# Optimization experiments

Hardware: AMD Instinct MI355X
Metric: run time of the kernel (lower is better)

The kernel has to match this reference:

```python
import jax, jax.numpy as jnp
import numpy as np

EPS = 1e-06


def elu_plus_one(x):
    # F.elu(x) + 1 == exp(x) for x < 0, x + 1 for x >= 0 (alpha=1)
    return jnp.where(x > 0, x + 1.0, jnp.exp(jnp.minimum(x, 0.0)))


def safe_divide(a, b, eps=EPS):
    return a / (b + eps)


def setup_inputs() -> dict:
    key0 = jax.random.key(0)
    kq, kk, kv, kM, kz = jax.random.split(key0, 5)
    B, H, S, D = 4, 16, 4096, 128
    query = jax.random.normal(kq, (B, H, S, D), dtype=jnp.float32)
    key = jax.random.normal(kk, (B, H, S, D), dtype=jnp.float32)
    value = jax.random.normal(kv, (B, H, S, D), dtype=jnp.float32)
    M = jax.random.normal(kM, (B, H, D, D), dtype=jnp.float32)
    z = jax.random.uniform(kz, (B, H, D, 1), dtype=jnp.float32)
    return {"query": query, "key": key, "value": value, "M": M, "z": z}


def reference(query, key, value, M, z):
    # --- update (delta rule) ---
    sigma_k = elu_plus_one(key)                       # [B,H,S,D]
    mem_pred = jnp.einsum('bhsd,bhde->bhse', sigma_k, M)   # sigma(K) @ M
    normalizer = jnp.einsum('bhsd,bhdo->bhso', sigma_k, z) # sigma(K) @ z -> [B,H,S,1]
    delta_v = value - safe_divide(mem_pred, normalizer)
    M_new = M + jnp.einsum('bhsd,bhse->bhde', sigma_k, delta_v)  # sigma(K)^T @ delta_V
    z_new = z + jnp.sum(sigma_k, axis=2)[..., None]              # [B,H,D,1]

    # --- retrieve with updated memory ---
    sigma_q = elu_plus_one(query)
    mem_out = jnp.einsum('bhsd,bhde->bhse', sigma_q, M_new)
    norm_q = jnp.einsum('bhsd,bhdo->bhso', sigma_q, z_new)
    out = safe_divide(mem_out, norm_q)                # [B,H,S,D]
    return out, M_new, z_new
```

## Files before the change

kernel.cpp:

```cpp
#include <hip/hip_runtime.h>
#include <math.h>

#define D 128
#define EPS 1e-6f
#define SKR_LD 136
#define SKT_LD 40

typedef __attribute__((ext_vector_type(8))) short short8;
typedef __attribute__((ext_vector_type(4))) float f32x4;
typedef unsigned short ushort_t;
typedef unsigned long long u64;

__device__ __forceinline__ float elu1(float x) {
    float e = __expf(fminf(x, 0.f));
    return x > 0.f ? x + 1.f : e;
}
__device__ __forceinline__ unsigned short bf16rne(float f) {
    unsigned u = __builtin_bit_cast(unsigned, f);
    u += 0x7FFFu + ((u >> 16) & 1u);
    return (unsigned short)(u >> 16);
}
__device__ __forceinline__ u64 pack4(float a, float b, float c, float d) {
    return (u64)bf16rne(a) | ((u64)bf16rne(b) << 16) |
           ((u64)bf16rne(c) << 32) | ((u64)bf16rne(d) << 48);
}

__global__ __launch_bounds__(256, 2)
void k_update(const float* __restrict__ key, const float* __restrict__ value,
              const float* __restrict__ M, const float* __restrict__ z,
              float* __restrict__ pM, float* __restrict__ pz, int S)
{
    __shared__ alignas(16) ushort_t skR[2][32 * SKR_LD];
    __shared__ alignas(16) ushort_t skT[2][128 * SKT_LD];
    __shared__ float normsh[2][32];
    __shared__ float zsc[8][128];

    const int t  = threadIdx.x;
    const int bh = blockIdx.x, ch = blockIdx.y, NCH = gridDim.y;
    const int SC = S / NCH;
    const int NB = SC / 32;
    const int s0g = ch * SC;

    const int w = t >> 6, g = (t >> 4) & 3, m = t & 15;
    const int sb = t >> 5, db = t & 31;

    const float* Kb = key   + (size_t)bh * S * D;
    const float* Vb = value + (size_t)bh * S * D;
    const float* Mb = M + (size_t)bh * D * D;
    const float* zb = z + (size_t)bh * D;

    float zr[4];
    #pragma unroll
    for (int j = 0; j < 4; ++j) zr[j] = zb[4 * db + j];

    short8 Bf[4][2];
    #pragma unroll
    for (int ks = 0; ks < 4; ++ks)
        #pragma unroll
        for (int p = 0; p < 2; ++p) {
            short8 f;
            #pragma unroll
            for (int j = 0; j < 8; ++j)
                f[j] = (short)bf16rne(Mb[(size_t)(32 * ks + 8 * g + j) * D + 16 * (2 * w + p) + m]);
            Bf[ks][p] = f;
        }

    f32x4 acc[8][2];
    #pragma unroll
    for (int dt = 0; dt < 8; ++dt)
        #pragma unroll
        for (int p = 0; p < 2; ++p) acc[dt][p] = 0.f;
    float zp[4] = {0.f, 0.f, 0.f, 0.f};

    auto STAGE_PROC = [&](const float4* kreg, int bu) {
        float sv[4][4];
        #pragma unroll
        for (int js = 0; js < 4; ++js) {
            sv[js][0] = elu1(kreg[js].x); sv[js][1] = elu1(kreg[js].y);
            sv[js][2] = elu1(kreg[js].z); sv[js][3] = elu1(kreg[js].w);
        }
        #pragma unroll
        for (int js = 0; js < 4; ++js)
            *(u64*)&skR[bu][(4 * sb + js) * SKR_LD + 4 * db] =
                pack4(sv[js][0], sv[js][1], sv[js][2], sv[js][3]);
        #pragma unroll
        for (int jd = 0; jd < 4; ++jd)
            *(u64*)&skT[bu][(4 * db + jd) * SKT_LD + 4 * sb] =
                pack4(sv[0][jd], sv[1][jd], sv[2][jd], sv[3][jd]);
        float np[4];
        #pragma unroll
        for (int js = 0; js < 4; ++js) {
            np[js] = sv[js][0] * zr[0] + sv[js][1] * zr[1] +
                     sv[js][2] * zr[2] + sv[js][3] * zr[3];
            #pragma unroll
            for (int jd = 0; jd < 4; ++jd) zp[jd] += sv[js][jd];
        }
        #pragma unroll
        for (int mask = 16; mask >= 1; mask >>= 1) {
            np[0] += __shfl_xor(np[0], mask, 64);
            np[1] += __shfl_xor(np[1], mask, 64);
            np[2] += __shfl_xor(np[2], mask, 64);
            np[3] += __shfl_xor(np[3], mask, 64);
        }
        if (db < 4) {
            float v = db == 0 ? np[0] : db == 1 ? np[1] : db == 2 ? np[2] : np[3];
            normsh[bu][4 * sb + db] = v + EPS;
        }
    };

    {
        float4 kreg[4];
        #pragma unroll
        for (int js = 0; js < 4; ++js)
            kreg[js] = *(const float4*)&Kb[(size_t)(s0g + 4 * sb + js) * D + 4 * db];
        STAGE_PROC(kreg, 0);
    }
    __syncthreads();

    for (int b = 0; b < NB; ++b) {
        const int bu = b & 1;
        float vv[2][2][4];
        #pragma unroll
        for (int st = 0; st < 2; ++st)
            #pragma unroll
            for (int p = 0; p < 2; ++p)
                #pragma unroll
                for (int r = 0; r < 4; ++r)
                    vv[st][p][r] = Vb[(size_t)(s0g + 32 * b + 16 * st + 4 * g + r) * D +
                                      16 * (2 * w + p) + m];
        float4 kreg[4];
        if (b + 1 < NB) {
            #pragma unroll
            for (int js = 0; js < 4; ++js)
                kreg[js] = *(const float4*)&Kb[(size_t)(s0g + 32 * (b + 1) + 4 * sb + js) * D + 4 * db];
        }

        f32x4 mp[2][2];
        #pragma unroll
        for (int st = 0; st < 2; ++st)
            #pragma unroll
            for (int p = 0; p < 2; ++p) mp[st][p] = 0.f;
        #pragma unroll
        for (int st = 0; st < 2; ++st)
            #pragma unroll
            for (int ks = 0; ks < 4; ++ks) {
                short8 a = *(short8*)&skR[bu][(16 * st + m) * SKR_LD + 32 * ks + 8 * g];
                #pragma unroll
                for (int p = 0; p < 2; ++p)
                    mp[st][p] = __builtin_amdgcn_mfma_f32_16x16x32_bf16(a, Bf[ks][p], mp[st][p], 0, 0, 0);
            }

        float dvv[2][2][4];
        #pragma unroll
        for (int st = 0; st < 2; ++st)
            #pragma unroll
            for (int r = 0; r < 4; ++r) {
                float nrm = normsh[bu][16 * st + 4 * g + r];
                #pragma unroll
                for (int p = 0; p < 2; ++p)
                    dvv[st][p][r] = vv[st][p][r] - mp[st][p][r] / nrm;
            }

        short8 bfr[2];
        #pragma unroll
        for (int p = 0; p < 2; ++p) {
            short8 f;
            #pragma unroll
            for (int j = 0; j < 8; ++j) {
                int src = ((2 * g + (j >> 2)) & 3) * 16 + m;
                float v0 = __shfl(dvv[0][p][j & 3], src, 64);
                float v1 = __shfl(dvv[1][p][j & 3], src, 64);
                f[j] = (short)bf16rne(g < 2 ? v0 : v1);
            }
            bfr[p] = f;
        }

        #pragma unroll
        for (int dt = 0; dt < 8; ++dt) {
            short8 a = *(short8*)&skT[bu][(16 * dt + m) * SKT_LD + 8 * g];
            #pragma unroll
            for (int p = 0; p < 2; ++p)
                acc[dt][p] = __builtin_amdgcn_mfma_f32_16x16x32_bf16(a, bfr[p], acc[dt][p], 0, 0, 0);
        }

        if (b + 1 < NB) STAGE_PROC(kreg, (b + 1) & 1);
        __syncthreads();
    }

    float* pMb = pM + ((size_t)bh * NCH + ch) * (D * D);
    #pragma unroll
    for (int dt = 0; dt < 8; ++dt)
        #pragma unroll
        for (int p = 0; p < 2; ++p)
            #pragma unroll
            for (int r = 0; r < 4; ++r)
                pMb[(size_t)(16 * dt + 4 * g + r) * D + 16 * (2 * w + p) + m] = acc[dt][p][r];

    #pragma unroll
    for (int jd = 0; jd < 4; ++jd) zsc[sb][4 * db + jd] = zp[jd];
    __syncthreads();
    if (t < 128) {
        float a = 0.f;
        #pragma unroll
        for (int q = 0; q < 8; ++q) a += zsc[q][t];
        pz[((size_t)bh * NCH + ch) * D + t] = a;
    }
}

__global__ void k_reduce(const float* __restrict__ M, const float* __restrict__ z,
                         const float* __restrict__ pM, const float* __restrict__ pz,
                         float* __restrict__ Mnew, float* __restrict__ znew, int NCH)
{
    const int bh = blockIdx.x, sl = blockIdx.y, t = threadIdx.x;
    const size_t baseM = (size_t)bh * D * D;
    for (int i = sl * 2048 + t; i < (sl + 1) * 2048; i += 256) {
        float a = M[baseM + i];
        for (int c = 0; c < NCH; ++c) a += pM[((size_t)bh * NCH + c) * (D * D) + i];
        Mnew[baseM + i] = a;
    }
    if (sl == 0 && t < D) {
        float a = z[(size_t)bh * D + t];
        for (int c = 0; c < NCH; ++c) a += pz[((size_t)bh * NCH + c) * D + t];
        znew[(size_t)bh * D + t] = a;
    }
}

__global__ __launch_bounds__(256, 2)
void k_retrieve(const float* __restrict__ query, const float* __restrict__ Mnew,
                const float* __restrict__ znew, float* __restrict__ out, int S)
{
    __shared__ alignas(16) ushort_t sqR[2][32 * SKR_LD];
    __shared__ float normsh[2][32];

    const int t  = threadIdx.x;
    const int bh = blockIdx.x, ch = blockIdx.y, NCH = gridDim.y;
    const int SC = S / NCH;
    const int NB = SC / 32;
    const int s0g = ch * SC;

    const int w = t >> 6, g = (t >> 4) & 3, m = t & 15;
    const int sb = t >> 5, db = t & 31;

    const float* Qb = query + (size_t)bh * S * D;
    const float* Mb = Mnew + (size_t)bh * D * D;
    const float* zb = znew + (size_t)bh * D;
    float*       Ob = out + (size_t)bh * S * D;

    float zr[4];
    #pragma unroll
    for (int j = 0; j < 4; ++j) zr[j] = zb[4 * db + j];

    short8 Bf[4][2];
    #pragma unroll
    for (int ks = 0; ks < 4; ++ks)
        #pragma unroll
        for (int p = 0; p < 2; ++p) {
            short8 f;
            #pragma unroll
            for (int j = 0; j < 8; ++j)
                f[j] = (short)bf16rne(Mb[(size_t)(32 * ks + 8 * g + j) * D + 16 * (2 * w + p) + m]);
            Bf[ks][p] = f;
        }

    auto STAGE_PROC = [&](const float4* qreg, int bu) {
        float sv[4][4];
        #pragma unroll
        for (int js = 0; js < 4; ++js) {
            sv[js][0] = elu1(qreg[js].x); sv[js][1] = elu1(qreg[js].y);
            sv[js][2] = elu1(qreg[js].z); sv[js][3] = elu1(qreg[js].w);
        }
        #pragma unroll
        for (int js = 0; js < 4; ++js)
            *(u64*)&sqR[bu][(4 * sb + js) * SKR_LD + 4 * db] =
                pack4(sv[js][0], sv[js][1], sv[js][2], sv[js][3]);
        float np[4];
        #pragma unroll
        for (int js = 0; js < 4; ++js)
            np[js] = sv[js][0] * zr[0] + sv[js][1] * zr[1] +
                     sv[js][2] * zr[2] + sv[js][3] * zr[3];
        #pragma unroll
        for (int mask = 16; mask >= 1; mask >>= 1) {
            np[0] += __shfl_xor(np[0], mask, 64);
            np[1] += __shfl_xor(np[1], mask, 64);
            np[2] += __shfl_xor(np[2], mask, 64);
            np[3] += __shfl_xor(np[3], mask, 64);
        }
        if (db < 4) {
            float v = db == 0 ? np[0] : db == 1 ? np[1] : db == 2 ? np[2] : np[3];
            normsh[bu][4 * sb + db] = v + EPS;
        }
    };

    {
        float4 qreg[4];
        #pragma unroll
        for (int js = 0; js < 4; ++js)
            qreg[js] = *(const float4*)&Qb[(size_t)(s0g + 4 * sb + js) * D + 4 * db];
        STAGE_PROC(qreg, 0);
    }
    __syncthreads();

    for (int b = 0; b < NB; ++b) {
        const int bu = b & 1;
        float4 qreg[4];
        if (b + 1 < NB) {
            #pragma unroll
            for (int js = 0; js < 4; ++js)
                qreg[js] = *(const float4*)&Qb[(size_t)(s0g + 32 * (b + 1) + 4 * sb + js) * D + 4 * db];
        }

        f32x4 mp[2][2];
        #pragma unroll
        for (int st = 0; st < 2; ++st)
            #pragma unroll
            for (int p = 0; p < 2; ++p) mp[st][p] = 0.f;
        #pragma unroll
        for (int st = 0; st < 2; ++st)
            #pragma unroll
            for (int ks = 0; ks < 4; ++ks) {
                short8 a = *(short8*)&sqR[bu][(16 * st + m) * SKR_LD + 32 * ks + 8 * g];
                #pragma unroll
                for (int p = 0; p < 2; ++p)
                    mp[st][p] = __builtin_amdgcn_mfma_f32_16x16x32_bf16(a, Bf[ks][p], mp[st][p], 0, 0, 0);
            }

        #pragma unroll
        for (int st = 0; st < 2; ++st)
            #pragma unroll
            for (int r = 0; r < 4; ++r) {
                float rn = 1.f / normsh[bu][16 * st + 4 * g + r];
                #pragma unroll
                for (int p = 0; p < 2; ++p)
                    Ob[(size_t)(s0g + 32 * b + 16 * st + 4 * g + r) * D + 16 * (2 * w + p) + m] =
                        mp[st][p][r] * rn;
            }

        if (b + 1 < NB) STAGE_PROC(qreg, (b + 1) & 1);
        __syncthreads();
    }
}

extern "C" void kernel_launch(void* const* d_in, const int* in_sizes, int n_in,
                              void* d_out, int out_size, void* d_ws, size_t ws_size,
                              hipStream_t stream)
{
    const float* q = (const float*)d_in[0];
    const float* k = (const float*)d_in[1];
    const float* v = (const float*)d_in[2];
    const float* M = (const float*)d_in[3];
    const float* z = (const float*)d_in[4];

    const int BH = in_sizes[3] / (D * D);
    const int S  = in_sizes[0] / (BH * D);

    float* out  = (float*)d_out;
    float* Mnew = out + (size_t)BH * S * D;
    float* znew = Mnew + (size_t)BH * D * D;

    int NCH = 8;
    const size_t per_set = (size_t)BH * (D * D + D) * sizeof(float);
    while (NCH > 1 && (size_t)NCH * per_set > ws_size) NCH >>= 1;

    float* pM;
    float* pz;
    if ((size_t)NCH * per_set <= ws_size) {
        pM = (float*)d_ws;
        pz = pM + (size_t)NCH * BH * D * D;
    } else {
        NCH = 1;
        pM = Mnew;
        pz = znew;
    }

    dim3 gridA(BH, NCH);
    k_update<<<gridA, 256, 0, stream>>>(k, v, M, z, pM, pz, S);
    dim3 gridB(BH, 8);
    k_reduce<<<gridB, 256, 0, stream>>>(M, z, pM, pz, Mnew, znew, NCH);
    dim3 gridC(BH, 8);
    k_retrieve<<<gridC, 256, 0, stream>>>(q, Mnew, znew, out, S);
}
```

Measured before the change: 155.6 us.

## Use 512-thread update blocks with MFMA normalizer and LDS delta transpose

```diff
diff --git a/kernel.cpp b/kernel.cpp
--- a/kernel.cpp
+++ b/kernel.cpp
@@ -5,6 +5,9 @@
 #define EPS 1e-6f
 #define SKR_LD 136
 #define SKT_LD 40
+#define DV_LD  40
+#define SKR_SZ (32 * SKR_LD)
+#define SKT_SZ (128 * SKT_LD)
 
 typedef __attribute__((ext_vector_type(8))) short short8;
 typedef __attribute__((ext_vector_type(4))) float f32x4;
@@ -25,184 +28,137 @@
            ((u64)bf16rne(c) << 32) | ((u64)bf16rne(d) << 48);
 }
 
-__global__ __launch_bounds__(256, 2)
+__global__ __launch_bounds__(512, 4)
 void k_update(const float* __restrict__ key, const float* __restrict__ value,
               const float* __restrict__ M, const float* __restrict__ z,
               float* __restrict__ pM, float* __restrict__ pz, int S)
 {
-    __shared__ alignas(16) ushort_t skR[2][32 * SKR_LD];
-    __shared__ alignas(16) ushort_t skT[2][128 * SKT_LD];
-    __shared__ float normsh[2][32];
-    __shared__ float zsc[8][128];
+    __shared__ alignas(16) ushort_t skR[2 * SKR_SZ];
+    __shared__ alignas(16) ushort_t skT[2 * SKT_SZ];
+    __shared__ alignas(16) ushort_t dvT[128 * DV_LD];
 
     const int t  = threadIdx.x;
     const int bh = blockIdx.x, ch = blockIdx.y, NCH = gridDim.y;
-    const int SC = S / NCH;
-    const int NB = SC / 32;
-    const int s0g = ch * SC;
+    const int SC = S / NCH, NB = SC / 32, s0g = ch * SC;
 
     const int w = t >> 6, g = (t >> 4) & 3, m = t & 15;
-    const int sb = t >> 5, db = t & 31;
+    const int c2 = t & 63;
 
     const float* Kb = key   + (size_t)bh * S * D;
     const float* Vb = value + (size_t)bh * S * D;
     const float* Mb = M + (size_t)bh * D * D;
     const float* zb = z + (size_t)bh * D;
 
-    float zr[4];
-    #pragma unroll
-    for (int j = 0; j < 4; ++j) zr[j] = zb[4 * db + j];
-
-    short8 Bf[4][2];
-    #pragma unroll
-    for (int ks = 0; ks < 4; ++ks)
-        #pragma unroll
-        for (int p = 0; p < 2; ++p) {
-            short8 f;
-            #pragma unroll
-            for (int j = 0; j < 8; ++j)
-                f[j] = (short)bf16rne(Mb[(size_t)(32 * ks + 8 * g + j) * D + 16 * (2 * w + p) + m]);
-            Bf[ks][p] = f;
-        }
-
-    f32x4 acc[8][2];
+    short8 Bf[4], zf[4];
+    #pragma unroll
+    for (int ks = 0; ks < 4; ++ks) {
+        short8 f, zfr;
+        #pragma unroll
+        for (int j = 0; j < 8; ++j) {
+            f[j]   = (short)bf16rne(Mb[(size_t)(32 * ks + 8 * g + j) * D + 16 * w + m]);
+            zfr[j] = (short)bf16rne(zb[32 * ks + 8 * g + j]);
+        }
+        Bf[ks] = f; zf[ks] = zfr;
+    }
+
+    f32x4 acc[8];
+    #pragma unroll
+    for (int dt = 0; dt < 8; ++dt) acc[dt] = 0.f;
+    float zacc0 = 0.f, zacc1 = 0.f;
+
+    auto STAGE = [&](const float2* kr, int buf) {
+        float sv0[4], sv1[4];
+        #pragma unroll
+        for (int i = 0; i < 4; ++i) { sv0[i] = elu1(kr[i].x); sv1[i] = elu1(kr[i].y); }
+        #pragma unroll
+        for (int i = 0; i < 4; ++i)
+            *(unsigned*)&skR[buf * SKR_SZ + (4 * w + i) * SKR_LD + 2 * c2] =
+                (unsigned)bf16rne(sv0[i]) | ((unsigned)bf16rne(sv1[i]) << 16);
+        *(u64*)&skT[buf * SKT_SZ + (2 * c2) * SKT_LD + 4 * w] =
+            pack4(sv0[0], sv0[1], sv0[2], sv0[3]);
+        *(u64*)&skT[buf * SKT_SZ + (2 * c2 + 1) * SKT_LD + 4 * w] =
+            pack4(sv1[0], sv1[1], sv1[2], sv1[3]);
+        zacc0 += sv0[0] + sv0[1] + sv0[2] + sv0[3];
+        zacc1 += sv1[0] + sv1[1] + sv1[2] + sv1[3];
+    };
+
+    {
+        float2 kr[4];
+        #pragma unroll
+        for (int i = 0; i < 4; ++i)
+            kr[i] = *(const float2*)&Kb[(size_t)(s0g + 4 * w + i) * D + 2 * c2];
+        STAGE(kr, 0);
+    }
+    __syncthreads();
+
+    for (int b = 0; b < NB; ++b) {
+        const int cur = b & 1;
+        const int sbat = s0g + 32 * b;
+
+        float2 kr[4];
+        if (b + 1 < NB) {
+            #pragma unroll
+            for (int i = 0; i < 4; ++i)
+                kr[i] = *(const float2*)&Kb[(size_t)(sbat + 32 + 4 * w + i) * D + 2 * c2];
+        }
+
+        float vv[2][4];
+        #pragma unroll
+        for (int st = 0; st < 2; ++st)
+            #pragma unroll
+            for (int r = 0; r < 4; ++r)
+                vv[st][r] = Vb[(size_t)(sbat + 16 * st + 4 * g + r) * D + 16 * w + m];
+
+        f32x4 mp[2], mz[2];
+        #pragma unroll
+        for (int st = 0; st < 2; ++st) { mp[st] = 0.f; mz[st] = 0.f; }
+        #pragma unroll
+        for (int st = 0; st < 2; ++st)
+            #pragma unroll
+            for (int ks = 0; ks < 4; ++ks) {
+                short8 a = *(short8*)&skR[cur * SKR_SZ + (16 * st + m) * SKR_LD + 32 * ks + 8 * g];
+                mp[st] = __builtin_amdgcn_mfma_f32_16x16x32_bf16(a, Bf[ks], mp[st], 0, 0, 0);
+                mz[st] = __builtin_amdgcn_mfma_f32_16x16x32_bf16(a, zf[ks], mz[st], 0, 0, 0);
+            }
+
+        #pragma unroll
+        for (int st = 0; st < 2; ++st) {
+            float dv[4];
+            #pragma unroll
+            for (int r = 0; r < 4; ++r)
+                dv[r] = vv[st][r] - mp[st][r] / (mz[st][r] + EPS);
+            *(u64*)&dvT[(16 * w + m) * DV_LD + 16 * st + 4 * g] =
+                pack4(dv[0], dv[1], dv[2], dv[3]);
+        }
+        asm volatile("" ::: "memory");
+
+        short8 bfr = *(short8*)&dvT[(16 * w + m) * DV_LD + 8 * g];
+
+        #pragma unroll
+        for (int dt = 0; dt < 8; ++dt) {
+            short8 a2 = *(short8*)&skT[cur * SKT_SZ + (16 * dt + m) * SKT_LD + 8 * g];
+            acc[dt] = __builtin_amdgcn_mfma_f32_16x16x32_bf16(a2, bfr, acc[dt], 0, 0, 0);
+        }
+
+        if (b + 1 < NB) STAGE(kr, cur ^ 1);
+        __syncthreads();
+    }
+
+    float* pMb = pM + ((size_t)bh * NCH + ch) * (D * D);
     #pragma unroll
     for (int dt = 0; dt < 8; ++dt)
         #pragma unroll
-        for (int p = 0; p < 2; ++p) acc[dt][p] = 0.f;
-    float zp[4] = {0.f, 0.f, 0.f, 0.f};
-
-    auto STAGE_PROC = [&](const float4* kreg, int bu) {
-        float sv[4][4];
-        #pragma unroll
-        for (int js = 0; js < 4; ++js) {
-            sv[js][0] = elu1(kreg[js].x); sv[js][1] = elu1(kreg[js].y);
-            sv[js][2] = elu1(kreg[js].z); sv[js][3] = elu1(kreg[js].w);
-        }
-        #pragma unroll
-        for (int js = 0; js < 4; ++js)
-            *(u64*)&skR[bu][(4 * sb + js) * SKR_LD + 4 * db] =
-                pack4(sv[js][0], sv[js][1], sv[js][2], sv[js][3]);
-        #pragma unroll
-        for (int jd = 0; jd < 4; ++jd)
-            *(u64*)&skT[bu][(4 * db + jd) * SKT_LD + 4 * sb] =
-                pack4(sv[0][jd], sv[1][jd], sv[2][jd], sv[3][jd]);
-        float np[4];
-        #pragma unroll
-        for (int js = 0; js < 4; ++js) {
-            np[js] = sv[js][0] * zr[0] + sv[js][1] * zr[1] +
-                     sv[js][2] * zr[2] + sv[js][3] * zr[3];
-            #pragma unroll
-            for (int jd = 0; jd < 4; ++jd) zp[jd] += sv[js][jd];
-        }
-        #pragma unroll
-        for (int mask = 16; mask >= 1; mask >>= 1) {
-            np[0] += __shfl_xor(np[0], mask, 64);
-            np[1] += __shfl_xor(np[1], mask, 64);
-            np[2] += __shfl_xor(np[2], mask, 64);
-            np[3] += __shfl_xor(np[3], mask, 64);
-        }
-        if (db < 4) {
-            float v = db == 0 ? np[0] : db == 1 ? np[1] : db == 2 ? np[2] : np[3];
-            normsh[bu][4 * sb + db] = v + EPS;
-        }
-    };
-
-    {
-        float4 kreg[4];
-        #pragma unroll
-        for (int js = 0; js < 4; ++js)
-            kreg[js] = *(const float4*)&Kb[(size_t)(s0g + 4 * sb + js) * D + 4 * db];
-        STAGE_PROC(kreg, 0);
-    }
-    __syncthreads();
-
-    for (int b = 0; b < NB; ++b) {
-        const int bu = b & 1;
-        float vv[2][2][4];
-        #pragma unroll
-        for (int st = 0; st < 2; ++st)
-            #pragma unroll
-            for (int p = 0; p < 2; ++p)
-                #pragma unroll
-                for (int r = 0; r < 4; ++r)
-                    vv[st][p][r] = Vb[(size_t)(s0g + 32 * b + 16 * st + 4 * g + r) * D +
-                                      16 * (2 * w + p) + m];
-        float4 kreg[4];
-        if (b + 1 < NB) {
-            #pragma unroll
-            for (int js = 0; js < 4; ++js)
-                kreg[js] = *(const float4*)&Kb[(size_t)(s0g + 32 * (b + 1) + 4 * sb + js) * D + 4 * db];
-        }
-
-        f32x4 mp[2][2];
-        #pragma unroll
-        for (int st = 0; st < 2; ++st)
-            #pragma unroll
-            for (int p = 0; p < 2; ++p) mp[st][p] = 0.f;
-        #pragma unroll
-        for (int st = 0; st < 2; ++st)
-            #pragma unroll
-            for (int ks = 0; ks < 4; ++ks) {
-                short8 a = *(short8*)&skR[bu][(16 * st + m) * SKR_LD + 32 * ks + 8 * g];
-                #pragma unroll
-                for (int p = 0; p < 2; ++p)
-                    mp[st][p] = __builtin_amdgcn_mfma_f32_16x16x32_bf16(a, Bf[ks][p], mp[st][p], 0, 0, 0);
-            }
-
-        float dvv[2][2][4];
-        #pragma unroll
-        for (int st = 0; st < 2; ++st)
-            #pragma unroll
-            for (int r = 0; r < 4; ++r) {
-                float nrm = normsh[bu][16 * st + 4 * g + r];
-                #pragma unroll
-                for (int p = 0; p < 2; ++p)
-                    dvv[st][p][r] = vv[st][p][r] - mp[st][p][r] / nrm;
-            }
-
-        short8 bfr[2];
-        #pragma unroll
-        for (int p = 0; p < 2; ++p) {
-            short8 f;
-            #pragma unroll
-            for (int j = 0; j < 8; ++j) {
-                int src = ((2 * g + (j >> 2)) & 3) * 16 + m;
-                float v0 = __shfl(dvv[0][p][j & 3], src, 64);
-                float v1 = __shfl(dvv[1][p][j & 3], src, 64);
-                f[j] = (short)bf16rne(g < 2 ? v0 : v1);
-            }
-            bfr[p] = f;
-        }
-
-        #pragma unroll
-        for (int dt = 0; dt < 8; ++dt) {
-            short8 a = *(short8*)&skT[bu][(16 * dt + m) * SKT_LD + 8 * g];
-            #pragma unroll
-            for (int p = 0; p < 2; ++p)
-                acc[dt][p] = __builtin_amdgcn_mfma_f32_16x16x32_bf16(a, bfr[p], acc[dt][p], 0, 0, 0);
-        }
-
-        if (b + 1 < NB) STAGE_PROC(kreg, (b + 1) & 1);
-        __syncthreads();
-    }
-
-    float* pMb = pM + ((size_t)bh * NCH + ch) * (D * D);
-    #pragma unroll
-    for (int dt = 0; dt < 8; ++dt)
-        #pragma unroll
-        for (int p = 0; p < 2; ++p)
-            #pragma unroll
-            for (int r = 0; r < 4; ++r)
-                pMb[(size_t)(16 * dt + 4 * g + r) * D + 16 * (2 * w + p) + m] = acc[dt][p][r];
-
-    #pragma unroll
-    for (int jd = 0; jd < 4; ++jd) zsc[sb][4 * db + jd] = zp[jd];
+        for (int r = 0; r < 4; ++r)
+            pMb[(size_t)(16 * dt + 4 * g + r) * D + 16 * w + m] = acc[dt][r];
+
+    float* zsc = (float*)skR;
+    zsc[w * 128 + 2 * c2]     = zacc0;
+    zsc[w * 128 + 2 * c2 + 1] = zacc1;
     __syncthreads();
     if (t < 128) {
         float a = 0.f;
         #pragma unroll
-        for (int q = 0; q < 8; ++q) a += zsc[q][t];
+        for (int r = 0; r < 8; ++r) a += zsc[r * 128 + t];
         pz[((size_t)bh * NCH + ch) * D + t] = a;
     }
 }
@@ -373,7 +329,7 @@
     }
 
     dim3 gridA(BH, NCH);
-    k_update<<<gridA, 256, 0, stream>>>(k, v, M, z, pM, pz, S);
+    k_update<<<gridA, 512, 0, stream>>>(k, v, M, z, pM, pz, S);
     dim3 gridB(BH, 8);
     k_reduce<<<gridB, 256, 0, stream>>>(M, z, pM, pz, Mnew, znew, NCH);
     dim3 gridC(BH, 8);
```

Result: no change. 157.4 us (+1.1%).
